# Kernel tuning notes

Hardware: AMD Instinct MI355X
Metric: run time of the kernel (lower is better)

## Reference

```python
import jax, jax.numpy as jnp
import numpy as np

EMBED_DIM = 512
NUM_HEADS = 8
GAMMA = 0.1


def setup_inputs() -> dict:
    key = jax.random.key(0)
    ks = jax.random.split(key, 16)
    B, T, D, Hp, Wp = 4, 16, EMBED_DIM, 24, 24
    Dq = D // 4
    s = 1.0 / np.sqrt(D)
    inp = {
        "h_opt": jax.random.normal(ks[0], (B, T, D, Hp, Wp), jnp.float32),
        "h_sar": jax.random.normal(ks[1], (B, T, D, Hp, Wp), jnp.float32),
        "Wq": jax.random.normal(ks[2], (D, D), jnp.float32) * s,
        "bq": jnp.zeros((D,), jnp.float32),
        "Wk": jax.random.normal(ks[3], (D, D), jnp.float32) * s,
        "bk": jnp.zeros((D,), jnp.float32),
        "Wv": jax.random.normal(ks[4], (D, D), jnp.float32) * s,
        "bv": jnp.zeros((D,), jnp.float32),
        "Wo": jax.random.normal(ks[5], (D, D), jnp.float32) * s,
        "bo": jnp.zeros((D,), jnp.float32),
        "Wp1": jax.random.normal(ks[6], (D, Dq), jnp.float32) * s,
        "bp1": jnp.zeros((Dq,), jnp.float32),
        "Wp2": jax.random.normal(ks[7], (Dq, 1), jnp.float32) * (1.0 / np.sqrt(Dq)),
        "bp2": jnp.zeros((1,), jnp.float32),
    }
    return inp


def reference(h_opt, h_sar, Wq, bq, Wk, bk, Wv, bv, Wo, bo, Wp1, bp1, Wp2, bp2):
    B, T, D, Hp, Wp_ = h_opt.shape
    S = Hp * Wp_
    H = NUM_HEADS
    hd = D // H

    # (B,T,D,H',W') -> (B*S, T, D): each spatial location is an independent sequence over T
    opt_seq = jnp.transpose(h_opt, (0, 3, 4, 1, 2)).reshape(B * S, T, D)
    sar_seq = jnp.transpose(h_sar, (0, 3, 4, 1, 2)).reshape(B * S, T, D)

    Q = (opt_seq @ Wq + bq).reshape(B * S, T, H, hd)
    K = (sar_seq @ Wk + bk).reshape(B * S, T, H, hd)
    V = (sar_seq @ Wv + bv).reshape(B * S, T, H, hd)

    # scores: (N, H, Tq, Tk)
    scores = jnp.einsum("nthd,nshd->nhts", Q, K) / np.sqrt(hd).astype(np.float32)

    # per-key physical violation penalty: MLP(sar) -> sigmoid in [0,1], shape (N, Tk)
    hdn = jax.nn.gelu(sar_seq @ Wp1 + bp1, approximate=False)
    p_viol = jax.nn.sigmoid((hdn @ Wp2 + bp2).squeeze(-1))  # (N, T)
    scores = scores - GAMMA * p_viol[:, None, None, :]

    attn = jax.nn.softmax(scores, axis=-1)  # dropout is identity in eval mode
    out = jnp.einsum("nhts,nshd->nthd", attn, V).reshape(B * S, T, D)
    out = out @ Wo + bo
    return jnp.transpose(out.reshape(B, Hp, Wp_, T, D), (0, 3, 4, 1, 2))
```

## Files before the change

### kernel.cpp

```cpp
#include <hip/hip_runtime.h>

#define GAMMA 0.1f

typedef unsigned short u16;
typedef u16 u16x8 __attribute__((ext_vector_type(8)));
typedef short s16x8 __attribute__((ext_vector_type(8)));
typedef float f32x4 __attribute__((ext_vector_type(4)));
typedef unsigned int ui32x4 __attribute__((ext_vector_type(4)));

__device__ __forceinline__ float b2f(u16 u) {
  return __uint_as_float(((unsigned)u) << 16);
}
__device__ __forceinline__ u16 f2bf(float f) {
  unsigned u = __float_as_uint(f);
  unsigned r = (u + 0x7FFFu + ((u >> 16) & 1u)) >> 16;
  return (u16)r;
}
__device__ __forceinline__ unsigned pk_bf16(float lo, float hi) {
  return (unsigned)f2bf(lo) | ((unsigned)f2bf(hi) << 16);
}

__device__ __forceinline__ void gl2lds16(const u16* g, u16* l) {
  __builtin_amdgcn_global_load_lds(
      (const __attribute__((address_space(1))) unsigned int*)g,
      (__attribute__((address_space(3))) unsigned int*)l, 16, 0, 0);
}

__device__ __forceinline__ int xcd_swz(int phys, int nwg) {
  return (phys & 7) * (nwg >> 3) + (phys >> 3);
}

#define PREP_NCONV 9216
#define PREP_T0 9216
#define PREP_T1 10240
#define PREP_T2 11264
#define PREP_T3 12288
#define PREP_T4 12544
#define PREP_T5 13568
#define PREP_NB 13577

__device__ __forceinline__ void tr_block(
    const float* __restrict__ src, u16* __restrict__ dst, int N, int blk, int tid)
{
  int idx = blk * 256 + tid;
  int nn = idx >> 9, kk = idx & 511;
  dst[idx] = f2bf(src[kk * N + nn]);
}

__global__ __launch_bounds__(256) void prep_all(
    const float* __restrict__ h0, const float* __restrict__ h1,
    u16* __restrict__ d0, u16* __restrict__ d1,
    const float* __restrict__ Wq, const float* __restrict__ Wk,
    const float* __restrict__ Wv, const float* __restrict__ Wp1,
    const float* __restrict__ Wo,
    const float* __restrict__ bq, const float* __restrict__ bk,
    const float* __restrict__ bv, const float* __restrict__ bp1,
    const float* __restrict__ bo,
    u16* __restrict__ WqT, u16* __restrict__ KVPW, u16* __restrict__ WoT,
    float* __restrict__ biasQ, float* __restrict__ biasKVP,
    float* __restrict__ biasO)
{
  __shared__ __align__(16) u16 T[64 * 64];
  const int b = blockIdx.x;
  const int tid = threadIdx.x;

  if (b < PREP_NCONV) {
    const int z = b / 4608;
    const int r_ = b - z * 4608;
    const int bt = r_ / 72;
    const int xx = r_ - bt * 72;
    const int kt = xx & 7, st = xx >> 3;
    const float* src = (z ? h1 : h0) + (size_t)bt * (512 * 576);
    u16* dst = (z ? d1 : d0) + (size_t)bt * (576 * 512);

    const int s = tid & 63, kc = tid >> 6;
    const float* sp = src + (size_t)(kt * 64 + kc * 16) * 576 + st * 64 + s;
    unsigned pk[8];
#pragma unroll
    for (int i = 0; i < 8; ++i) {
      float lo = sp[(2 * i) * 576];
      float hi = sp[(2 * i + 1) * 576];
      pk[i] = pk_bf16(lo, hi);
    }
    ui32x4 v0 = {pk[0], pk[1], pk[2], pk[3]};
    ui32x4 v1 = {pk[4], pk[5], pk[6], pk[7]};
    *(ui32x4*)&T[s * 64 + (((kc * 2)     ^ (s & 7)) * 8)] = v0;
    *(ui32x4*)&T[s * 64 + (((kc * 2 + 1) ^ (s & 7)) * 8)] = v1;
    __syncthreads();
    const int r = tid >> 2, oc = (tid & 3) * 2;
    ui32x4 w0 = *(const ui32x4*)&T[r * 64 + ((oc       ^ (r & 7)) * 8)];
    ui32x4 w1 = *(const ui32x4*)&T[r * 64 + (((oc + 1) ^ (r & 7)) * 8)];
    u16* dp = dst + (size_t)(st * 64 + r) * 512 + kt * 64 + oc * 8;
    *(ui32x4*)dp = w0;
    *(ui32x4*)(dp + 8) = w1;
  } else if (b < PREP_T1) {
    tr_block(Wq, WqT, 512, b - PREP_T0, tid);
  } else if (b < PREP_T2) {
    tr_block(Wk, KVPW, 512, b - PREP_T1, tid);
  } else if (b < PREP_T3) {
    tr_block(Wv, KVPW + 512 * 512, 512, b - PREP_T2, tid);
  } else if (b < PREP_T4) {
    tr_block(Wp1, KVPW + 1024 * 512, 128, b - PREP_T3, tid);
  } else if (b < PREP_T5) {
    tr_block(Wo, WoT, 512, b - PREP_T4, tid);
  } else {
    int i = (b - PREP_T5) * 256 + tid;
    if (i < 512) {
      biasQ[i] = bq[i];
    } else if (i < 1664) {
      int j = i - 512;
      float v;
      if (j < 512) v = bk[j];
      else if (j < 1024) v = bv[j - 512];
      else v = bp1[j - 1024];
      biasKVP[j] = v;
    } else if (i < 2176) {
      biasO[i - 1664] = bo[i - 1664];
    }
  }
}

__global__ __launch_bounds__(256) void gemm_proj_all(
    const u16* __restrict__ hTopt, const u16* __restrict__ hTsar,
    const u16* __restrict__ WqT, const u16* __restrict__ KVPW,
    const float* __restrict__ biasQ, const float* __restrict__ biasKVP,
    const float* __restrict__ Wp2, const float* __restrict__ bp2,
    u16* __restrict__ Qbuf, u16* __restrict__ KVPbuf,
    float* __restrict__ pviol)
{
  __shared__ __align__(16) u16 Al[2][64 * 64];
  __shared__ __align__(16) u16 Bl[2][128 * 64];
  __shared__ float Pv[256];
  const int tid = threadIdx.x;
  const int w = tid >> 6, lane = tid & 63;
  const int lhi = lane >> 4, llo = lane & 15;

  const int nwg = 13 * 576;
  const int phys = blockIdx.y * 13 + blockIdx.x;
  const int logical = xcd_swz(phys, nwg);
  const int bx = logical % 13;
  const int y = logical / 13;

  const int bt = y / 9, stile = y - bt * 9;
  const int s0 = stile * 64;

  const bool isQ = (bx < 4);
  const int bxl = isQ ? bx : bx - 4;
  const int col0 = bxl * 128;
  const int NC = isQ ? 512 : 1152;
  const u16* Ab = (isQ ? hTopt : hTsar) + (size_t)bt * (576 * 512)
                  + (size_t)s0 * 512;
  const u16* Bb = (isQ ? WqT : KVPW) + (size_t)col0 * 512;
  const float* bias = isQ ? biasQ : biasKVP;
  u16* C = isQ ? Qbuf : KVPbuf;
  const bool dopv = (!isQ) && (bxl == 8);

  const int brow = lane >> 3;
  const int bko = ((lane & 7) ^ brow) * 8;

  f32x4 acc[4][2];
#pragma unroll
  for (int mi = 0; mi < 4; ++mi)
#pragma unroll
    for (int ni = 0; ni < 2; ++ni)
#pragma unroll
      for (int e = 0; e < 4; ++e) acc[mi][ni][e] = 0.f;

#pragma unroll
  for (int i = 0; i < 2; ++i) {
    int q = w * 2 + i;
    gl2lds16(Ab + (size_t)(q * 8 + brow) * 512 + bko, &Al[0][q * 512]);
  }
#pragma unroll
  for (int i = 0; i < 4; ++i) {
    int q = w * 4 + i;
    gl2lds16(Bb + (size_t)(q * 8 + brow) * 512 + bko, &Bl[0][q * 512]);
  }

  for (int kt = 0; kt < 8; ++kt) {
    __syncthreads();
    if (kt < 7) {
      const int ktn = kt + 1;
#pragma unroll
      for (int i = 0; i < 2; ++i) {
        int q = w * 2 + i;
        gl2lds16(Ab + (size_t)(q * 8 + brow) * 512 + ktn * 64 + bko,
                 &Al[ktn & 1][q * 512]);
      }
#pragma unroll
      for (int i = 0; i < 4; ++i) {
        int q = w * 4 + i;
        gl2lds16(Bb + (size_t)(q * 8 + brow) * 512 + ktn * 64 + bko,
                 &Bl[ktn & 1][q * 512]);
      }
    }
    const u16* Alc = Al[kt & 1];
    const u16* Blc = Bl[kt & 1];
#pragma unroll
    for (int hh = 0; hh < 2; ++hh) {
      s16x8 af[4], bfr[2];
#pragma unroll
      for (int mi = 0; mi < 4; ++mi) {
        int row = mi * 16 + llo;
        af[mi] = *(const s16x8*)&Alc[row * 64 + ((((hh << 2) | lhi) ^ (row & 7)) * 8)];
      }
#pragma unroll
      for (int ni = 0; ni < 2; ++ni) {
        int n = w * 32 + ni * 16 + llo;
        bfr[ni] = *(const s16x8*)&Blc[n * 64 + ((((hh << 2) | lhi) ^ (n & 7)) * 8)];
      }
#pragma unroll
      for (int mi = 0; mi < 4; ++mi)
#pragma unroll
        for (int ni = 0; ni < 2; ++ni)
          acc[mi][ni] = __builtin_amdgcn_mfma_f32_16x16x32_bf16(
              af[mi], bfr[ni], acc[mi][ni], 0, 0, 0);
    }
  }

  const int b_ = bt >> 4, t_ = bt & 15;
  const size_t rowbase = (size_t)(b_ * 576 + s0) * 16 + t_;
  float bia0 = bias[col0 + w * 32 + llo];
  float bia1 = bias[col0 + w * 32 + 16 + llo];

  if (dopv) {
    const float w2a = Wp2[w * 32 + llo];
    const float w2b = Wp2[w * 32 + 16 + llo];
    float part[16];
#pragma unroll
    for (int mi = 0; mi < 4; ++mi)
#pragma unroll
      for (int i = 0; i < 4; ++i) {
        float x0 = acc[mi][0][i] + bia0;
        float x1 = acc[mi][1][i] + bia1;
        float g0 = 0.5f * x0 * (1.f + erff(x0 * 0.70710678f));
        float g1 = 0.5f * x1 * (1.f + erff(x1 * 0.70710678f));
        part[mi * 4 + i] = g0 * w2a + g1 * w2b;
      }
#pragma unroll
    for (int d = 1; d < 16; d <<= 1)
#pragma unroll
      for (int idx = 0; idx < 16; ++idx)
        part[idx] += __shfl_xor(part[idx], d, 64);
    if (llo == 0) {
#pragma unroll
      for (int mi = 0; mi < 4; ++mi)
#pragma unroll
        for (int i = 0; i < 4; ++i)
          Pv[w * 64 + mi * 16 + lhi * 4 + i] = part[mi * 4 + i];
    }
    __syncthreads();
    if (tid < 64) {
      float sum = Pv[tid] + Pv[64 + tid] + Pv[128 + tid] + Pv[192 + tid]
                  + bp2[0];
      pviol[rowbase + (size_t)tid * 16] = 1.f / (1.f + expf(-sum));
    }
  } else {
#pragma unroll
    for (int mi = 0; mi < 4; ++mi) {
#pragma unroll
      for (int i = 0; i < 4; ++i) {
        const int m = mi * 16 + lhi * 4 + i;
        u16* cp = C + (rowbase + (size_t)m * 16) * NC + col0 + w * 32 + llo;
        cp[0]  = f2bf(acc[mi][0][i] + bia0);
        cp[16] = f2bf(acc[mi][1][i] + bia1);
      }
    }
  }
}

__global__ __launch_bounds__(256) void attn_kernel(
    const u16* Q, const u16* __restrict__ KVP,
    const float* __restrict__ pviol, u16* att)
{
  __shared__ __align__(16) u16 Kl[4][16 * 72];
  __shared__ __align__(16) u16 Vl[4][16 * 72];
  __shared__ float Pl[4][16 * 17];
  const int tid = threadIdx.x;
  const int w = tid >> 6, lane = tid & 63;
  const int logical = xcd_swz(blockIdx.x, gridDim.x);
  const int wid = logical * 4 + w;
  const int n = wid >> 3, hh = wid & 7;
  const int g = lane >> 4, tq = lane & 15;

  const int r = lane >> 3, co = (lane & 7) * 8;
  const u16* Kb = KVP + (size_t)n * (16 * 1152) + hh * 64;
#pragma unroll
  for (int rr = 0; rr < 2; ++rr) {
    int row = r + rr * 8;
    *(u16x8*)&Kl[w][row * 72 + co] = *(const u16x8*)(Kb + row * 1152 + co);
    *(u16x8*)&Vl[w][row * 72 + co] = *(const u16x8*)(Kb + 512 + row * 1152 + co);
  }
  __syncthreads();

  float s[4] = {0.f, 0.f, 0.f, 0.f};
  const u16* Qr = Q + ((size_t)n * 16 + tq) * 512 + hh * 64;
  for (int kc = 0; kc < 8; ++kc) {
    u16x8 q8 = *(const u16x8*)(Qr + kc * 8);
    float qf[8];
#pragma unroll
    for (int j = 0; j < 8; ++j) qf[j] = b2f(q8[j]);
#pragma unroll
    for (int i = 0; i < 4; ++i) {
      u16x8 k8 = *(const u16x8*)&Kl[w][(g * 4 + i) * 72 + kc * 8];
#pragma unroll
      for (int j = 0; j < 8; ++j) s[i] += qf[j] * b2f(k8[j]);
    }
  }

  const float* pv = pviol + n * 16;
#pragma unroll
  for (int i = 0; i < 4; ++i) s[i] = s[i] * 0.125f - GAMMA * pv[g * 4 + i];

  float mx = fmaxf(fmaxf(s[0], s[1]), fmaxf(s[2], s[3]));
  mx = fmaxf(mx, __shfl_xor(mx, 16, 64));
  mx = fmaxf(mx, __shfl_xor(mx, 32, 64));
  float e[4], sum = 0.f;
#pragma unroll
  for (int i = 0; i < 4; ++i) { e[i] = expf(s[i] - mx); sum += e[i]; }
  sum += __shfl_xor(sum, 16, 64);
  sum += __shfl_xor(sum, 32, 64);
  float inv = 1.f / sum;
#pragma unroll
  for (int i = 0; i < 4; ++i) Pl[w][tq * 17 + g * 4 + i] = e[i] * inv;
  __syncthreads();

  float o[16];
#pragma unroll
  for (int j = 0; j < 16; ++j) o[j] = 0.f;
  for (int tk = 0; tk < 16; ++tk) {
    float p = Pl[w][tq * 17 + tk];
    u16x8 v0 = *(const u16x8*)&Vl[w][tk * 72 + g * 16];
    u16x8 v1 = *(const u16x8*)&Vl[w][tk * 72 + g * 16 + 8];
#pragma unroll
    for (int j = 0; j < 8; ++j) {
      o[j]     += p * b2f(v0[j]);
      o[8 + j] += p * b2f(v1[j]);
    }
  }
  u16* op = att + ((size_t)n * 16 + tq) * 512 + hh * 64 + g * 16;
  u16x8 r0, r1;
#pragma unroll
  for (int j = 0; j < 8; ++j) { r0[j] = f2bf(o[j]); r1[j] = f2bf(o[8 + j]); }
  *(u16x8*)op = r0;
  *(u16x8*)(op + 8) = r1;
}

__global__ __launch_bounds__(256) void gemm_out(
    const u16* __restrict__ A, const u16* __restrict__ WT,
    const float* __restrict__ bias, float* __restrict__ out)
{
  __shared__ __align__(16) char smem[49152];
  u16* Al0 = (u16*)smem;
  u16* Bl0 = (u16*)(smem + 16384);
  const int tid = threadIdx.x;
  const int w = tid >> 6, lane = tid & 63;
  const int lhi = lane >> 4, llo = lane & 15;

  const int nwg = gridDim.x * gridDim.y;
  const int phys = blockIdx.y * gridDim.x + blockIdx.x;
  const int logical = xcd_swz(phys, nwg);
  const int bx = logical % gridDim.x;
  const int y = logical / gridDim.x;

  const int bt = y / 9, stile = y - bt * 9;
  const int s0 = stile * 64;
  const int col0 = bx * 128;
  const int b_ = bt >> 4, t_ = bt & 15;

  const u16* Ab = A + ((size_t)(b_ * 576 + s0) * 16 + t_) * 512;
  const u16* Bb = WT + (size_t)col0 * 512;

  const int brow = lane >> 3;
  const int bko = ((lane & 7) ^ brow) * 8;

  f32x4 acc[4][2];
#pragma unroll
  for (int mi = 0; mi < 4; ++mi)
#pragma unroll
    for (int ni = 0; ni < 2; ++ni)
#pragma unroll
      for (int e = 0; e < 4; ++e) acc[mi][ni][e] = 0.f;

#pragma unroll
  for (int i = 0; i < 2; ++i) {
    int q = w * 2 + i;
    gl2lds16(Ab + (size_t)(q * 8 + brow) * (16 * 512) + bko, &Al0[q * 512]);
  }
#pragma unroll
  for (int i = 0; i < 4; ++i) {
    int q = w * 4 + i;
    gl2lds16(Bb + (size_t)(q * 8 + brow) * 512 + bko, &Bl0[q * 512]);
  }

  for (int kt = 0; kt < 8; ++kt) {
    __syncthreads();
    if (kt < 7) {
      const int ktn = kt + 1;
      u16* Ala = Al0 + (ktn & 1) * (64 * 64);
      u16* Bla = Bl0 + (ktn & 1) * (128 * 64);
#pragma unroll
      for (int i = 0; i < 2; ++i) {
        int q = w * 2 + i;
        gl2lds16(Ab + (size_t)(q * 8 + brow) * (16 * 512) + ktn * 64 + bko,
                 &Ala[q * 512]);
      }
#pragma unroll
      for (int i = 0; i < 4; ++i) {
        int q = w * 4 + i;
        gl2lds16(Bb + (size_t)(q * 8 + brow) * 512 + ktn * 64 + bko,
                 &Bla[q * 512]);
      }
    }
    const u16* Alc = Al0 + (kt & 1) * (64 * 64);
    const u16* Blc = Bl0 + (kt & 1) * (128 * 64);
#pragma unroll
    for (int hh = 0; hh < 2; ++hh) {
      s16x8 af[4], bfr[2];
#pragma unroll
      for (int mi = 0; mi < 4; ++mi) {
        int row = mi * 16 + llo;
        af[mi] = *(const s16x8*)&Alc[row * 64 + ((((hh << 2) | lhi) ^ (row & 7)) * 8)];
      }
#pragma unroll
      for (int ni = 0; ni < 2; ++ni) {
        int n = w * 32 + ni * 16 + llo;
        bfr[ni] = *(const s16x8*)&Blc[n * 64 + ((((hh << 2) | lhi) ^ (n & 7)) * 8)];
      }
#pragma unroll
      for (int mi = 0; mi < 4; ++mi)
#pragma unroll
        for (int ni = 0; ni < 2; ++ni)
          acc[mi][ni] = __builtin_amdgcn_mfma_f32_16x16x32_bf16(
              af[mi], bfr[ni], acc[mi][ni], 0, 0, 0);
    }
  }

  __syncthreads();
  float* Cl = (float*)smem;
  float bia0 = bias[col0 + w * 32 + llo];
  float bia1 = bias[col0 + w * 32 + 16 + llo];
#pragma unroll
  for (int mi = 0; mi < 4; ++mi)
#pragma unroll
    for (int i = 0; i < 4; ++i) {
      int m = mi * 16 + lhi * 4 + i;
      Cl[(w * 32 + llo) * 72 + m]      = acc[mi][0][i] + bia0;
      Cl[(w * 32 + 16 + llo) * 72 + m] = acc[mi][1][i] + bia1;
    }
  __syncthreads();
  const int nn = tid >> 1;
  const int mh = (tid & 1) * 32;
  const float* sp = Cl + nn * 72 + mh;
  float* dp = out + ((size_t)bt * 512 + col0 + nn) * 576 + s0 + mh;
#pragma unroll
  for (int j = 0; j < 8; ++j)
    *(float4*)(dp + j * 4) = *(const float4*)(sp + j * 4);
}

extern "C" void kernel_launch(void* const* d_in, const int* in_sizes, int n_in,
                              void* d_out, int out_size, void* d_ws, size_t ws_size,
                              hipStream_t stream)
{
  const float* h_opt = (const float*)d_in[0];
  const float* h_sar = (const float*)d_in[1];
  const float* Wq  = (const float*)d_in[2];
  const float* bq  = (const float*)d_in[3];
  const float* Wk  = (const float*)d_in[4];
  const float* bk  = (const float*)d_in[5];
  const float* Wv  = (const float*)d_in[6];
  const float* bv  = (const float*)d_in[7];
  const float* Wo  = (const float*)d_in[8];
  const float* bo  = (const float*)d_in[9];
  const float* Wp1 = (const float*)d_in[10];
  const float* bp1 = (const float*)d_in[11];
  const float* Wp2 = (const float*)d_in[12];
  const float* bp2 = (const float*)d_in[13];
  float* out = (float*)d_out;

  char* ws = (char*)d_ws;
  u16*   WqT     = (u16*)(ws + 0);
  u16*   KVPW    = (u16*)(ws + 524288);
  u16*   WoT     = (u16*)(ws + 1703936);
  float* biasQ   = (float*)(ws + 2228224);
  float* biasKVP = (float*)(ws + 2230272);
  float* biasO   = (float*)(ws + 2234880);
  float* pviol   = (float*)(ws + 2236928);
  u16*   Qbuf    = (u16*)(ws + 2384384);
  u16*   KVPbuf  = (u16*)(ws + 40133120);
  u16*   hTopt   = (u16*)(ws + 125067776);
  u16*   hTsar   = (u16*)(ws + 162816512);

  prep_all<<<PREP_NB, 256, 0, stream>>>(
      h_opt, h_sar, hTopt, hTsar, Wq, Wk, Wv, Wp1, Wo,
      bq, bk, bv, bp1, bo, WqT, KVPW, WoT, biasQ, biasKVP, biasO);

  gemm_proj_all<<<dim3(13, 576), 256, 0, stream>>>(
      hTopt, hTsar, WqT, KVPW, biasQ, biasKVP, Wp2, bp2,
      Qbuf, KVPbuf, pviol);

  attn_kernel<<<4608, 256, 0, stream>>>(Qbuf, KVPbuf, pviol, Qbuf);
  gemm_out<<<dim3(4, 576), 256, 0, stream>>>(Qbuf, WoT, biasO, out);
}
```

Baseline: 408.0 us.

## Use MFMA for attention QK^T and PV, drop block syncs

Rewrites the per-head attention kernel to compute scores with two bf16 16x16x32 MFMAs reading Q and K straight from global memory. It then builds a P fragment with lane shuffles and computes P·V with MFMAs using zero-padded K. Block-wide __syncthreads are removed because each wave only touches its own LDS slice, and the output is staged through LDS so stores are coalesced. It also rounds P to bf16 before the PV product, which adds precision loss, and relies on correct MFMA lane layout reasoning.

```diff
diff --git a/kernel.cpp b/kernel.cpp
--- a/kernel.cpp
+++ b/kernel.cpp
@@ -273,44 +273,41 @@
     const u16* Q, const u16* __restrict__ KVP,
     const float* __restrict__ pviol, u16* att)
 {
-  __shared__ __align__(16) u16 Kl[4][16 * 72];
   __shared__ __align__(16) u16 Vl[4][16 * 72];
-  __shared__ float Pl[4][16 * 17];
+  __shared__ __align__(16) u16 Ol[4][16 * 72];
   const int tid = threadIdx.x;
   const int w = tid >> 6, lane = tid & 63;
   const int logical = xcd_swz(blockIdx.x, gridDim.x);
   const int wid = logical * 4 + w;
   const int n = wid >> 3, hh = wid & 7;
-  const int g = lane >> 4, tq = lane & 15;
+  const int g = lane >> 4, llo = lane & 15;
 
   const int r = lane >> 3, co = (lane & 7) * 8;
-  const u16* Kb = KVP + (size_t)n * (16 * 1152) + hh * 64;
-#pragma unroll
-  for (int rr = 0; rr < 2; ++rr) {
-    int row = r + rr * 8;
-    *(u16x8*)&Kl[w][row * 72 + co] = *(const u16x8*)(Kb + row * 1152 + co);
-    *(u16x8*)&Vl[w][row * 72 + co] = *(const u16x8*)(Kb + 512 + row * 1152 + co);
-  }
-  __syncthreads();
-
-  float s[4] = {0.f, 0.f, 0.f, 0.f};
-  const u16* Qr = Q + ((size_t)n * 16 + tq) * 512 + hh * 64;
-  for (int kc = 0; kc < 8; ++kc) {
-    u16x8 q8 = *(const u16x8*)(Qr + kc * 8);
-    float qf[8];
-#pragma unroll
-    for (int j = 0; j < 8; ++j) qf[j] = b2f(q8[j]);
-#pragma unroll
-    for (int i = 0; i < 4; ++i) {
-      u16x8 k8 = *(const u16x8*)&Kl[w][(g * 4 + i) * 72 + kc * 8];
-#pragma unroll
-      for (int j = 0; j < 8; ++j) s[i] += qf[j] * b2f(k8[j]);
-    }
-  }
+  {
+    const u16* Vb = KVP + (size_t)n * (16 * 1152) + 512 + hh * 64;
+#pragma unroll
+    for (int rr = 0; rr < 2; ++rr) {
+      int row = r + rr * 8;
+      *(u16x8*)&Vl[w][row * 72 + co] =
+          *(const u16x8*)(Vb + (size_t)row * 1152 + co);
+    }
+  }
+
+  const u16* Qr = Q + ((size_t)n * 16 + llo) * 512 + hh * 64;
+  const u16* Kr = KVP + ((size_t)n * 16 + llo) * 1152 + hh * 64;
+  s16x8 qa0 = *(const s16x8*)(Qr + g * 8);
+  s16x8 qa1 = *(const s16x8*)(Qr + 32 + g * 8);
+  s16x8 ka0 = *(const s16x8*)(Kr + g * 8);
+  s16x8 ka1 = *(const s16x8*)(Kr + 32 + g * 8);
+
+  f32x4 sacc = {0.f, 0.f, 0.f, 0.f};
+  sacc = __builtin_amdgcn_mfma_f32_16x16x32_bf16(ka0, qa0, sacc, 0, 0, 0);
+  sacc = __builtin_amdgcn_mfma_f32_16x16x32_bf16(ka1, qa1, sacc, 0, 0, 0);
 
   const float* pv = pviol + n * 16;
-#pragma unroll
-  for (int i = 0; i < 4; ++i) s[i] = s[i] * 0.125f - GAMMA * pv[g * 4 + i];
+  float s[4];
+#pragma unroll
+  for (int i = 0; i < 4; ++i) s[i] = sacc[i] * 0.125f - GAMMA * pv[g * 4 + i];
 
   float mx = fmaxf(fmaxf(s[0], s[1]), fmaxf(s[2], s[3]));
   mx = fmaxf(mx, __shfl_xor(mx, 16, 64));
@@ -321,29 +318,48 @@
   sum += __shfl_xor(sum, 16, 64);
   sum += __shfl_xor(sum, 32, 64);
   float inv = 1.f / sum;
-#pragma unroll
-  for (int i = 0; i < 4; ++i) Pl[w][tq * 17 + g * 4 + i] = e[i] * inv;
-  __syncthreads();
-
-  float o[16];
-#pragma unroll
-  for (int j = 0; j < 16; ++j) o[j] = 0.f;
-  for (int tk = 0; tk < 16; ++tk) {
-    float p = Pl[w][tq * 17 + tk];
-    u16x8 v0 = *(const u16x8*)&Vl[w][tk * 72 + g * 16];
-    u16x8 v1 = *(const u16x8*)&Vl[w][tk * 72 + g * 16 + 8];
-#pragma unroll
-    for (int j = 0; j < 8; ++j) {
-      o[j]     += p * b2f(v0[j]);
-      o[8 + j] += p * b2f(v1[j]);
-    }
-  }
-  u16* op = att + ((size_t)n * 16 + tq) * 512 + hh * 64 + g * 16;
-  u16x8 r0, r1;
-#pragma unroll
-  for (int j = 0; j < 8; ++j) { r0[j] = f2bf(o[j]); r1[j] = f2bf(o[8 + j]); }
-  *(u16x8*)op = r0;
-  *(u16x8*)(op + 8) = r1;
+
+  unsigned p01 = pk_bf16(e[0] * inv, e[1] * inv);
+  unsigned p23 = pk_bf16(e[2] * inv, e[3] * inv);
+
+  const int sa = ((2 * g) & 3) * 16 + llo;
+  const int sb = ((2 * g + 1) & 3) * 16 + llo;
+  unsigned a0 = (unsigned)__shfl((int)p01, sa, 64);
+  unsigned a1 = (unsigned)__shfl((int)p23, sa, 64);
+  unsigned b0 = (unsigned)__shfl((int)p01, sb, 64);
+  unsigned b1 = (unsigned)__shfl((int)p23, sb, 64);
+  ui32x4 afu = {0u, 0u, 0u, 0u};
+  if (g < 2) { afu[0] = a0; afu[1] = a1; afu[2] = b0; afu[3] = b1; }
+  s16x8 pfrag;
+  __builtin_memcpy(&pfrag, &afu, 16);
+
+  f32x4 oacc[4];
+#pragma unroll
+  for (int c = 0; c < 4; ++c) {
+    u16 vb[8];
+#pragma unroll
+    for (int j = 0; j < 8; ++j)
+      vb[j] = (g < 2) ? Vl[w][(g * 8 + j) * 72 + c * 16 + llo] : (u16)0;
+    s16x8 vfrag;
+    __builtin_memcpy(&vfrag, vb, 16);
+    f32x4 z = {0.f, 0.f, 0.f, 0.f};
+    oacc[c] = __builtin_amdgcn_mfma_f32_16x16x32_bf16(pfrag, vfrag, z, 0, 0, 0);
+  }
+
+#pragma unroll
+  for (int c = 0; c < 4; ++c)
+#pragma unroll
+    for (int i = 0; i < 4; ++i)
+      Ol[w][(g * 4 + i) * 72 + c * 16 + llo] = f2bf(oacc[c][i]);
+
+  {
+    u16* ob = att + ((size_t)n * 16) * 512 + hh * 64;
+#pragma unroll
+    for (int rr = 0; rr < 2; ++rr) {
+      int row = r + rr * 8;
+      *(u16x8*)(ob + (size_t)row * 512 + co) = *(const u16x8*)&Ol[w][row * 72 + co];
+    }
+  }
 }
 
 __global__ __launch_bounds__(256) void gemm_out(
```

After: 389.9 us. 4.4% less time.
